# Kernel optimization log

Hardware: AMD Instinct MI355X
Metric: run time of the kernel (lower is better)

## Reference

```python
import jax, jax.numpy as jnp
import numpy as np

B, M, K = 4096, 64, 3          # graphs, points per graph, knn k
FX, FP = 59, 3                 # node features, position dims (FX+FP = 62)
EPS = 1e-5


def _lin_init(key, fan_in, fan_out):
    k1, k2 = jax.random.split(key)
    s = 1.0 / np.sqrt(fan_in)
    W = jax.random.uniform(k1, (fan_in, fan_out), jnp.float32, -s, s)
    b = jax.random.uniform(k2, (fan_out,), jnp.float32, -s, s)
    return W, b


def setup_inputs() -> dict:
    key = jax.random.key(0)
    ks = jax.random.split(key, 8)
    x = jax.random.normal(ks[0], (B * M, FX), jnp.float32)
    pos = jax.random.normal(ks[1], (B * M, FP), jnp.float32)
    batch = jnp.repeat(jnp.arange(B, dtype=jnp.int32), M)
    W1, b1 = _lin_init(ks[2], FX + FP, 128)
    W2, b2 = _lin_init(ks[3], 128, 128)
    Wc1, bc1 = _lin_init(ks[4], 128, 256)
    Wc2, bc2 = _lin_init(ks[5], 256, 1)
    return dict(
        x=x, pos=pos, batch=batch,
        W1=W1, b1=b1, g1=jnp.ones(128), be1=jnp.zeros(128),
        W2=W2, b2=b2, g2=jnp.ones(128), be2=jnp.zeros(128),
        Wc1=Wc1, bc1=bc1, gc1=jnp.ones(256), bec1=jnp.zeros(256),
        Wc2=Wc2, bc2=bc2, gc2=jnp.ones(1), bec2=jnp.zeros(1),
    )


def _mlp_block(h, W, b, g, be):
    # Linear -> ReLU -> BatchNorm1d (training-mode batch statistics)
    h = jax.nn.relu(h @ W + b)
    mu = h.mean(axis=0)
    var = h.var(axis=0)  # biased, as torch BN uses for normalization
    return g * (h - mu) * jax.lax.rsqrt(var + EPS) + be


def _knn_idx(pos_b):
    # pos_b: [B, M, FP]; per-graph k-NN (loop=False)
    d = jnp.sum((pos_b[:, :, None, :] - pos_b[:, None, :, :]) ** 2, axis=-1)  # [B,M,M]
    d = d + jnp.eye(M, dtype=d.dtype) * 1e10  # exclude self-loops
    _, nbr = jax.lax.top_k(-d, K)  # [B, M, K] neighbor (source) indices
    return nbr


def reference(x, pos, batch, W1, b1, g1, be1, W2, b2, g2, be2,
              Wc1, bc1, gc1, bec1, Wc2, bc2, gc2, bec2):
    x_b = x.reshape(B, M, FX)
    pos_b = pos.reshape(B, M, FP)
    nbr = _knn_idx(pos_b)                                   # [B,M,K]
    # gather neighbor features and relative positions (edge messages)
    xj = jax.vmap(lambda xb, nb: xb[nb])(x_b, nbr)          # [B,M,K,FX]
    pj = jax.vmap(lambda pb, nb: pb[nb])(pos_b, nbr)        # [B,M,K,FP]
    rel = pj - pos_b[:, :, None, :]
    msg = jnp.concatenate([xj, rel], axis=-1).reshape(B * M * K, FX + FP)
    # local_nn on every edge, then max aggregation per target node
    h = _mlp_block(msg, W1, b1, g1, be1)                    # [E,128]
    h = h.reshape(B, M, K, 128).max(axis=2).reshape(B * M, 128)
    # global_nn per node
    h = _mlp_block(h, W2, b2, g2, be2)                      # [N,128]
    # global mean pool over graphs
    sums = jax.ops.segment_sum(h, batch, num_segments=B)
    cnt = jax.ops.segment_sum(jnp.ones((B * M,), h.dtype), batch, num_segments=B)
    pooled = sums / cnt[:, None]                            # [B,128]
    # classifier MLP([128,256,1])
    c = _mlp_block(pooled, Wc1, bc1, gc1, bec1)
    c = _mlp_block(c, Wc2, bc2, gc2, bec2)                  # [B,1]
    return jax.nn.sigmoid(c)[:, 0]
```

## Files before the change

### kernel.cpp

```cpp
#include <hip/hip_runtime.h>
#include <hip/hip_bf16.h>
#include <math.h>

#define NB   4096
#define MM   64
#define KNN  3
#define FX   59
#define H    128
#define NN   (NB*MM)
#define NE   (NN*KNN)
#define C1   256
#define EPSB 1e-5f
#define NSH  16

typedef __attribute__((ext_vector_type(8))) short short8;
typedef __attribute__((ext_vector_type(4))) float f32x4;

__device__ __forceinline__ float wave_red(float v) {
#pragma unroll
    for (int m = 32; m >= 1; m >>= 1) v += __shfl_xor(v, m, 64);
    return v;
}

__device__ __forceinline__ void atomAddF(float* p, float v) {
    __hip_atomic_fetch_add(p, v, __ATOMIC_RELAXED, __HIP_MEMORY_SCOPE_AGENT);
}

__device__ __forceinline__ unsigned short f2bf(float f) {
    union { float f; unsigned u; } v; v.f = f;
    unsigned r = v.u + 0x7fffu + ((v.u >> 16) & 1u);
    return (unsigned short)(r >> 16);
}

__device__ __forceinline__ unsigned int pack_bf2(float a, float b) {
    union { __hip_bfloat162 h; unsigned int u; } cv;
    cv.h = __float22bfloat162_rn(make_float2(a, b));
    return cv.u;
}

__global__ __launch_bounds__(512, 8) void k_knn_mfma1(
    const float* __restrict__ x, const float* __restrict__ pos,
    const float* __restrict__ W1, const float* __restrict__ b1,
    unsigned short* __restrict__ h1max,
    float* __restrict__ S1sh, float* __restrict__ Q1sh)
{
    __shared__ float pos_s[MM * 3];
    __shared__ int   nbr_s[MM * 3];
    __shared__ float b1_s[H];
    __shared__ float w1p_s[3 * H];
    __shared__ __align__(16) unsigned short a_s[MM * 72];
    __shared__ __align__(16) unsigned int   u_s32[MM * 66];

    const int blk = blockIdx.x, tid = threadIdx.x;
    const float* xg = x + (size_t)blk * MM * FX;
    const float* pg = pos + (size_t)blk * MM * 3;

    {
        const int node = tid >> 3, g = tid & 7;
        const int c0g = g * 8;
        float v[8];
#pragma unroll
        for (int i = 0; i < 8; ++i) {
            int cI = c0g + i;
            v[i] = (cI < FX) ? xg[node * FX + cI]
                             : ((cI < 62) ? pg[node * 3 + (cI - FX)] : 0.f);
        }
        uint4 pk;
        pk.x = pack_bf2(v[0], v[1]); pk.y = pack_bf2(v[2], v[3]);
        pk.z = pack_bf2(v[4], v[5]); pk.w = pack_bf2(v[6], v[7]);
        const int gs = (g + node) & 7;
        *(uint4*)(a_s + node * 72 + gs * 8) = pk;
    }
    if (tid < MM * 3) pos_s[tid] = pg[tid];
    if (tid < H) b1_s[tid] = b1[tid];
    if (tid < 3 * H) w1p_s[tid] = W1[(FX + (tid >> 7)) * H + (tid & 127)];

    const int lane = tid & 63;
    const int w    = tid >> 6;
    const int m    = lane & 15;
    const int kg   = lane >> 4;
    const int ch   = w * 16 + m;

    short8 bfr[2];
#pragma unroll
    for (int kc = 0; kc < 2; ++kc) {
        float t8[8];
#pragma unroll
        for (int i = 0; i < 8; ++i) {
            int k = kc * 32 + kg * 8 + i;
            t8[i] = (k < 62) ? W1[k * H + ch] : 0.f;
        }
        uint4 pk;
        pk.x = pack_bf2(t8[0], t8[1]); pk.y = pack_bf2(t8[2], t8[3]);
        pk.z = pack_bf2(t8[4], t8[5]); pk.w = pack_bf2(t8[6], t8[7]);
        bfr[kc] = *(short8*)&pk;
    }
    __syncthreads();

    {
        const int node = tid >> 3, q = tid & 7;
        const float px = pos_s[node * 3 + 0];
        const float py = pos_s[node * 3 + 1];
        const float pz = pos_s[node * 3 + 2];
        float d0 = 1e30f, d1 = 1e30f, d2 = 1e30f;
        int   i0 = 1 << 30, i1 = 1 << 30, i2 = 1 << 30;
        for (int jj = 0; jj < 8; ++jj) {
            int j = q * 8 + jj;
            if (j == node) continue;
            float dx = pos_s[j * 3 + 0] - px;
            float dy = pos_s[j * 3 + 1] - py;
            float dz = pos_s[j * 3 + 2] - pz;
            float d = dx * dx + dy * dy + dz * dz;
            bool b2v = (d < d2) || (d == d2 && j < i2);
            bool b1v = (d < d1) || (d == d1 && j < i1);
            bool b0v = (d < d0) || (d == d0 && j < i0);
            float nd2 = b1v ? d1 : d; int ni2 = b1v ? i1 : j;
            float nd1 = b0v ? d0 : d; int ni1 = b0v ? i0 : j;
            d2 = b2v ? nd2 : d2; i2 = b2v ? ni2 : i2;
            d1 = b1v ? nd1 : d1; i1 = b1v ? ni1 : i1;
            d0 = b0v ? d   : d0; i0 = b0v ? j   : i0;
        }
#pragma unroll
        for (int mq = 1; mq <= 4; mq <<= 1) {
            float e[3]; int f[3];
            e[0] = __shfl_xor(d0, mq, 64); f[0] = __shfl_xor(i0, mq, 64);
            e[1] = __shfl_xor(d1, mq, 64); f[1] = __shfl_xor(i1, mq, 64);
            e[2] = __shfl_xor(d2, mq, 64); f[2] = __shfl_xor(i2, mq, 64);
#pragma unroll
            for (int t3 = 0; t3 < 3; ++t3) {
                float ev = e[t3]; int fv = f[t3];
                bool b2v = (ev < d2) || (ev == d2 && fv < i2);
                bool b1v = (ev < d1) || (ev == d1 && fv < i1);
                bool b0v = (ev < d0) || (ev == d0 && fv < i0);
                float nd2 = b1v ? d1 : ev; int ni2 = b1v ? i1 : fv;
                float nd1 = b0v ? d0 : ev; int ni1 = b0v ? i0 : fv;
                d2 = b2v ? nd2 : d2; i2 = b2v ? ni2 : i2;
                d1 = b1v ? nd1 : d1; i1 = b1v ? ni1 : i1;
                d0 = b0v ? ev  : d0; i0 = b0v ? fv  : i0;
            }
        }
        if (q == 0) {
            nbr_s[node * 3 + 0] = i0;
            nbr_s[node * 3 + 1] = i1;
            nbr_s[node * 3 + 2] = i2;
        }
    }

    f32x4 acc[4];
#pragma unroll
    for (int rt = 0; rt < 4; ++rt) acc[rt] = (f32x4){0.f, 0.f, 0.f, 0.f};

#pragma unroll
    for (int kc = 0; kc < 2; ++kc)
#pragma unroll
        for (int rt = 0; rt < 4; ++rt) {
            const int row = rt * 16 + m;
            const int gs = ((kc * 4 + kg) + row) & 7;
            short8 a = *(const short8*)(a_s + row * 72 + gs * 8);
            acc[rt] = __builtin_amdgcn_mfma_f32_16x16x32_bf16(bfr[kc], a, acc[rt], 0, 0, 0);
        }
#pragma unroll
    for (int rt = 0; rt < 4; ++rt) {
        int node = rt * 16 + m;
        int pidx = 8 * w + 2 * kg;
        uint2 val;
        val.x = pack_bf2(acc[rt][0], acc[rt][1]);
        val.y = pack_bf2(acc[rt][2], acc[rt][3]);
        *(uint2*)(u_s32 + node * 66 + pidx) = val;
    }
    __syncthreads();

    const int c0 = 2 * lane, c1v = 2 * lane + 1;
    const float wpa0 = w1p_s[c0],      wpa1 = w1p_s[H + c0],  wpa2 = w1p_s[2 * H + c0];
    const float wpb0 = w1p_s[c1v],     wpb1 = w1p_s[H + c1v], wpb2 = w1p_s[2 * H + c1v];
    const float b1a = b1_s[c0], b1b = b1_s[c1v];
    float s0 = 0.f, s1 = 0.f, q0 = 0.f, q1 = 0.f;
    unsigned int* hout32 = (unsigned int*)(h1max + (size_t)blk * MM * H);
#pragma unroll
    for (int ii = 0; ii < 8; ++ii) {
        int node = w * 8 + ii;
        int j0 = nbr_s[node * 3 + 0];
        int j1 = nbr_s[node * 3 + 1];
        int j2 = nbr_s[node * 3 + 2];
        float px = pos_s[node * 3 + 0], py = pos_s[node * 3 + 1], pz = pos_s[node * 3 + 2];
        float basea = b1a - (px * wpa0 + py * wpa1 + pz * wpa2);
        float baseb = b1b - (px * wpb0 + py * wpb1 + pz * wpb2);
        unsigned int v0 = u_s32[j0 * 66 + lane];
        unsigned int v1 = u_s32[j1 * 66 + lane];
        unsigned int v2 = u_s32[j2 * 66 + lane];
        float h0a = fmaxf(__uint_as_float(v0 << 16) + basea, 0.f);
        float h1a = fmaxf(__uint_as_float(v1 << 16) + basea, 0.f);
        float h2a = fmaxf(__uint_as_float(v2 << 16) + basea, 0.f);
        float h0b = fmaxf(__uint_as_float(v0 & 0xffff0000u) + baseb, 0.f);
        float h1b = fmaxf(__uint_as_float(v1 & 0xffff0000u) + baseb, 0.f);
        float h2b = fmaxf(__uint_as_float(v2 & 0xffff0000u) + baseb, 0.f);
        s0 += h0a + h1a + h2a; q0 += h0a * h0a + h1a * h1a + h2a * h2a;
        s1 += h0b + h1b + h2b; q1 += h0b * h0b + h1b * h1b + h2b * h2b;
        float ma = fmaxf(fmaxf(h0a, h1a), h2a);
        float mb = fmaxf(fmaxf(h0b, h1b), h2b);
        hout32[node * 64 + lane] = pack_bf2(ma, mb);
    }
    __syncthreads();

    float* s_red = (float*)a_s;
    float* q_red = (float*)u_s32;
    *(float2*)(s_red + w * 128 + c0) = make_float2(s0, s1);
    *(float2*)(q_red + w * 128 + c0) = make_float2(q0, q1);
    __syncthreads();
    const int sel = blk & (NSH - 1);
    if (tid < 128) {
        float S = 0.f;
#pragma unroll
        for (int ww = 0; ww < 8; ++ww) S += s_red[ww * 128 + tid];
        atomAddF(&S1sh[sel * H + tid], S);
    } else if (tid < 256) {
        int t2 = tid - 128;
        float Q = 0.f;
#pragma unroll
        for (int ww = 0; ww < 8; ++ww) Q += q_red[ww * 128 + t2];
        atomAddF(&Q1sh[sel * H + t2], Q);
    }
}

__global__ __launch_bounds__(128) void k_prep2(
    const float* __restrict__ W2, const float* __restrict__ S1sh,
    const float* __restrict__ Q1sh, const float* __restrict__ g1,
    const float* __restrict__ be1, const float* __restrict__ b2,
    unsigned short* __restrict__ W2t, float* __restrict__ b2p)
{
    const int n = blockIdx.x, k = threadIdx.x;
    float S = 0.f, Q = 0.f;
#pragma unroll
    for (int i = 0; i < NSH; ++i) { S += S1sh[i * H + k]; Q += Q1sh[i * H + k]; }
    float mu  = S * (1.f / (float)NE);
    float var = Q * (1.f / (float)NE) - mu * mu;
    float a   = g1[k] * rsqrtf(var + EPSB);
    float cc  = be1[k] - mu * a;
    float wv  = W2[k * H + n];
    W2t[n * H + k] = f2bf(a * wv);
    float contrib = wave_red(cc * wv);
    __shared__ float red2[2];
    if ((k & 63) == 0) red2[k >> 6] = contrib;
    __syncthreads();
    if (k == 0) b2p[n] = b2[n] + red2[0] + red2[1];
}

__global__ __launch_bounds__(256) void k_mfma2(
    const unsigned short* __restrict__ h1max, const unsigned short* __restrict__ W2t,
    const float* __restrict__ b2p,
    float* __restrict__ graphsum, float* __restrict__ S2sh, float* __restrict__ Q2sh)
{
    __shared__ __align__(16) unsigned short a_s[MM * 136];
    const int blk = blockIdx.x, tid = threadIdx.x;
    const unsigned short* hg = h1max + (size_t)blk * MM * H;
    for (int t = tid; t < MM * H / 8; t += 256) {
        int row = t >> 4, col8 = (t & 15) * 8;
        *(short8*)(a_s + row * 136 + col8) = *(const short8*)(hg + row * H + col8);
    }
    __syncthreads();

    const int lane = tid & 63, w = tid >> 6, wcol = w * 32;
    const int m = lane & 15, kg = lane >> 4;

    short8 bfr[2][4];
#pragma unroll
    for (int ct = 0; ct < 2; ++ct)
#pragma unroll
        for (int kc = 0; kc < 4; ++kc)
            bfr[ct][kc] = *(const short8*)(W2t + (wcol + ct * 16 + m) * H + kc * 32 + kg * 8);

    f32x4 acc[4][2];
#pragma unroll
    for (int rt = 0; rt < 4; ++rt)
#pragma unroll
        for (int ct = 0; ct < 2; ++ct) acc[rt][ct] = (f32x4){0.f, 0.f, 0.f, 0.f};

#pragma unroll
    for (int kc = 0; kc < 4; ++kc)
#pragma unroll
        for (int rt = 0; rt < 4; ++rt) {
            short8 a = *(const short8*)(a_s + (rt * 16 + m) * 136 + kc * 32 + kg * 8);
#pragma unroll
            for (int ct = 0; ct < 2; ++ct)
                acc[rt][ct] = __builtin_amdgcn_mfma_f32_16x16x32_bf16(a, bfr[ct][kc], acc[rt][ct], 0, 0, 0);
        }

    const int sel = blk & (NSH - 1);
#pragma unroll
    for (int ct = 0; ct < 2; ++ct) {
        float bv = b2p[wcol + ct * 16 + m];
        float s = 0.f, q = 0.f;
#pragma unroll
        for (int rt = 0; rt < 4; ++rt)
#pragma unroll
            for (int r = 0; r < 4; ++r) {
                float v = fmaxf(acc[rt][ct][r] + bv, 0.f);
                s += v; q += v * v;
            }
        s += __shfl_xor(s, 16, 64); q += __shfl_xor(q, 16, 64);
        s += __shfl_xor(s, 32, 64); q += __shfl_xor(q, 32, 64);
        if (lane < 16) {
            int col = wcol + ct * 16 + lane;
            graphsum[(size_t)blk * H + col] = s;
            atomAddF(&S2sh[sel * H + col], s);
            atomAddF(&Q2sh[sel * H + col], q);
        }
    }
}

__global__ __launch_bounds__(256) void k_cls1(
    const float* __restrict__ graphsum,
    const float* __restrict__ S2sh, const float* __restrict__ Q2sh,
    const float* __restrict__ g2, const float* __restrict__ be2,
    const float* __restrict__ Wc1, const float* __restrict__ bc1,
    float* __restrict__ c1raw, float* __restrict__ S3, float* __restrict__ Q3)
{
    __shared__ float a2_s[H], c2_s[H];
    const int blk = blockIdx.x, tid = threadIdx.x;
    if (tid < H) {
        float S = 0.f, Q = 0.f;
#pragma unroll
        for (int i = 0; i < NSH; ++i) { S += S2sh[i * H + tid]; Q += Q2sh[i * H + tid]; }
        float mu  = S * (1.f / (float)NN);
        float var = Q * (1.f / (float)NN) - mu * mu;
        float a   = g2[tid] * rsqrtf(var + EPSB);
        a2_s[tid] = a;
        c2_s[tid] = be2[tid] - mu * a;
    }
    __syncthreads();
    __shared__ float pooled_s[16 * H];
    const int g0 = blk * 16;
    for (int t = tid; t < 16 * H; t += 256) {
        int f = t & 127;
        pooled_s[t] = a2_s[f] * (graphsum[(size_t)g0 * H + t] * (1.f / 64.f)) + c2_s[f];
    }
    __syncthreads();
    const int c = tid;
    float acc[16];
    const float bias = bc1[c];
#pragma unroll
    for (int gi = 0; gi < 16; ++gi) acc[gi] = bias;
    for (int f = 0; f < H; ++f) {
        float wv = Wc1[f * C1 + c];
#pragma unroll
        for (int gi = 0; gi < 16; ++gi) acc[gi] += pooled_s[gi * H + f] * wv;
    }
    float s = 0.f, q = 0.f;
#pragma unroll
    for (int gi = 0; gi < 16; ++gi) {
        float h = fmaxf(acc[gi], 0.f);
        c1raw[(size_t)(g0 + gi) * C1 + c] = h;
        s += h; q += h * h;
    }
    atomAddF(&S3[c], s);
    atomAddF(&Q3[c], q);
}

__global__ __launch_bounds__(256) void k_cls2(
    const float* __restrict__ c1raw,
    const float* __restrict__ S3, const float* __restrict__ Q3,
    const float* __restrict__ gc1, const float* __restrict__ bec1,
    const float* __restrict__ Wc2, const float* __restrict__ bc2,
    float* __restrict__ z, float* __restrict__ SzQz)
{
    __shared__ float a3_s[C1], c3_s[C1], w3_s[C1];
    __shared__ float zloc[16];
    const int blk = blockIdx.x, tid = threadIdx.x;
    {
        float S = S3[tid], Q = Q3[tid];
        float mu  = S * (1.f / (float)NB);
        float var = Q * (1.f / (float)NB) - mu * mu;
        float a   = gc1[tid] * rsqrtf(var + EPSB);
        a3_s[tid] = a;
        c3_s[tid] = bec1[tid] - mu * a;
        w3_s[tid] = Wc2[tid];
    }
    __syncthreads();
    const int g0 = blk * 16;
    {
        const int gi = tid >> 4, part = tid & 15;
        const float* crow = c1raw + (size_t)(g0 + gi) * C1 + part * 16;
        float acc3 = 0.f;
#pragma unroll
        for (int i = 0; i < 16; i += 4) {
            float4 cv = *(const float4*)(crow + i);
            int f = part * 16 + i;
            acc3 += (a3_s[f + 0] * cv.x + c3_s[f + 0]) * w3_s[f + 0];
            acc3 += (a3_s[f + 1] * cv.y + c3_s[f + 1]) * w3_s[f + 1];
            acc3 += (a3_s[f + 2] * cv.z + c3_s[f + 2]) * w3_s[f + 2];
            acc3 += (a3_s[f + 3] * cv.w + c3_s[f + 3]) * w3_s[f + 3];
        }
#pragma unroll
        for (int mm = 1; mm <= 8; mm <<= 1) acc3 += __shfl_xor(acc3, mm, 64);
        if (part == 0) zloc[gi] = fmaxf(acc3 + bc2[0], 0.f);
    }
    __syncthreads();
    if (tid < 16) z[g0 + tid] = zloc[tid];
    if (tid == 0) {
        float s = 0.f, q = 0.f;
#pragma unroll
        for (int i = 0; i < 16; ++i) { float zz = zloc[i]; s += zz; q += zz * zz; }
        atomAddF(&SzQz[0], s);
        atomAddF(&SzQz[1], q);
    }
}

__global__ __launch_bounds__(256) void k_final(
    const float* __restrict__ z, const float* __restrict__ SzQz,
    const float* __restrict__ gc2, const float* __restrict__ bec2,
    float* __restrict__ out)
{
    const int g = blockIdx.x * 256 + threadIdx.x;
    float S = SzQz[0], Q = SzQz[1];
    float mu  = S * (1.f / 4096.f);
    float var = Q * (1.f / 4096.f) - mu * mu;
    float a   = gc2[0] * rsqrtf(var + EPSB);
    float cb  = bec2[0] - mu * a;
    float v = a * z[g] + cb;
    out[g] = 1.f / (1.f + expf(-v));
}

extern "C" void kernel_launch(void* const* d_in, const int* in_sizes, int n_in,
                              void* d_out, int out_size, void* d_ws, size_t ws_size,
                              hipStream_t stream)
{
    const float* x    = (const float*)d_in[0];
    const float* pos  = (const float*)d_in[1];
    const float* W1   = (const float*)d_in[3];
    const float* b1   = (const float*)d_in[4];
    const float* g1   = (const float*)d_in[5];
    const float* be1  = (const float*)d_in[6];
    const float* W2   = (const float*)d_in[7];
    const float* b2   = (const float*)d_in[8];
    const float* g2   = (const float*)d_in[9];
    const float* be2  = (const float*)d_in[10];
    const float* Wc1  = (const float*)d_in[11];
    const float* bc1  = (const float*)d_in[12];
    const float* gc1  = (const float*)d_in[13];
    const float* bec1 = (const float*)d_in[14];
    const float* Wc2  = (const float*)d_in[15];
    const float* bc2  = (const float*)d_in[16];
    const float* gc2  = (const float*)d_in[17];
    const float* bec2 = (const float*)d_in[18];
    float* out = (float*)d_out;

    float* ws = (float*)d_ws;
    size_t off = 0;
    auto alloc = [&](size_t n) { float* p = ws + off; off += n; return p; };
    unsigned short* h1max = (unsigned short*)alloc((size_t)NN * H / 2);
    unsigned short* W2t   = (unsigned short*)alloc(128 * 128 / 2);
    float* b2p     = alloc(H);
    float* graphsum= alloc((size_t)NB * H);
    float* c1raw   = alloc((size_t)NB * C1);
    float* zbuf    = alloc(NB);
    const size_t ATOMN = (size_t)4 * NSH * H + 2 * C1 + 2;
    float* atomics = alloc(ATOMN);
    float* S1sh = atomics;
    float* Q1sh = S1sh + NSH * H;
    float* S2sh = Q1sh + NSH * H;
    float* Q2sh = S2sh + NSH * H;
    float* S3   = Q2sh + NSH * H;
    float* Q3   = S3 + C1;
    float* SzQz = Q3 + C1;

    hipMemsetAsync(atomics, 0, ATOMN * sizeof(float), stream);
    k_knn_mfma1<<<dim3(NB), dim3(512), 0, stream>>>(x, pos, W1, b1, h1max, S1sh, Q1sh);
    k_prep2<<<dim3(128), dim3(128), 0, stream>>>(W2, S1sh, Q1sh, g1, be1, b2, W2t, b2p);
    k_mfma2<<<dim3(NB), dim3(256), 0, stream>>>(h1max, W2t, b2p, graphsum, S2sh, Q2sh);
    k_cls1<<<dim3(256), dim3(256), 0, stream>>>(graphsum, S2sh, Q2sh, g2, be2, Wc1, bc1, c1raw, S3, Q3);
    k_cls2<<<dim3(256), dim3(256), 0, stream>>>(c1raw, S3, Q3, gc1, bec1, Wc2, bc2, zbuf, SzQz);
    k_final<<<dim3(16), dim3(256), 0, stream>>>(zbuf, SzQz, gc2, bec2, out);
}
```

Measured before the change: 254.4 us.

## Gather edge rows into LDS and run MFMA per edge instead of per node

```diff
diff --git a/kernel.cpp b/kernel.cpp
--- a/kernel.cpp
+++ b/kernel.cpp
@@ -47,17 +47,15 @@
     __shared__ float pos_s[MM * 3];
     __shared__ int   nbr_s[MM * 3];
     __shared__ float b1_s[H];
-    __shared__ float w1p_s[3 * H];
     __shared__ __align__(16) unsigned short a_s[MM * 72];
-    __shared__ __align__(16) unsigned int   u_s32[MM * 66];
+    __shared__ __align__(16) unsigned short e_s[3 * MM * 72];
 
     const int blk = blockIdx.x, tid = threadIdx.x;
     const float* xg = x + (size_t)blk * MM * FX;
     const float* pg = pos + (size_t)blk * MM * 3;
 
     {
-        const int node = tid >> 3, g = tid & 7;
-        const int c0g = g * 8;
+        const int node = tid >> 3, c0g = (tid & 7) * 8;
         float v[8];
 #pragma unroll
         for (int i = 0; i < 8; ++i) {
@@ -68,12 +66,10 @@
         uint4 pk;
         pk.x = pack_bf2(v[0], v[1]); pk.y = pack_bf2(v[2], v[3]);
         pk.z = pack_bf2(v[4], v[5]); pk.w = pack_bf2(v[6], v[7]);
-        const int gs = (g + node) & 7;
-        *(uint4*)(a_s + node * 72 + gs * 8) = pk;
+        *(uint4*)(a_s + node * 72 + c0g) = pk;
     }
     if (tid < MM * 3) pos_s[tid] = pg[tid];
     if (tid < H) b1_s[tid] = b1[tid];
-    if (tid < 3 * H) w1p_s[tid] = W1[(FX + (tid >> 7)) * H + (tid & 127)];
 
     const int lane = tid & 63;
     const int w    = tid >> 6;
@@ -145,79 +141,96 @@
             nbr_s[node * 3 + 2] = i2;
         }
     }
-
-    f32x4 acc[4];
-#pragma unroll
-    for (int rt = 0; rt < 4; ++rt) acc[rt] = (f32x4){0.f, 0.f, 0.f, 0.f};
-
-#pragma unroll
-    for (int kc = 0; kc < 2; ++kc)
-#pragma unroll
-        for (int rt = 0; rt < 4; ++rt) {
-            const int row = rt * 16 + m;
-            const int gs = ((kc * 4 + kg) + row) & 7;
-            short8 a = *(const short8*)(a_s + row * 72 + gs * 8);
-            acc[rt] = __builtin_amdgcn_mfma_f32_16x16x32_bf16(bfr[kc], a, acc[rt], 0, 0, 0);
-        }
-#pragma unroll
-    for (int rt = 0; rt < 4; ++rt) {
-        int node = rt * 16 + m;
-        int pidx = 8 * w + 2 * kg;
+    __syncthreads();
+
+#pragma unroll
+    for (int it = 0; it < 3; ++it) {
+        const int T = tid + it * 512;
+        const int row = T >> 3, g = T & 7;
+        const int node = row & 63, slot = row >> 6;
+        const int j = nbr_s[node * 3 + slot];
+        if (g < 7) {
+            *(uint4*)(e_s + row * 72 + g * 8) = *(const uint4*)(a_s + j * 72 + g * 8);
+        } else {
+            uint4 v = *(const uint4*)(a_s + j * 72 + 56);
+            float r0 = pos_s[j * 3 + 0] - pos_s[node * 3 + 0];
+            float r1 = pos_s[j * 3 + 1] - pos_s[node * 3 + 1];
+            float r2 = pos_s[j * 3 + 2] - pos_s[node * 3 + 2];
+            v.y = (v.y & 0xffffu) | ((unsigned)f2bf(r0) << 16);
+            v.z = pack_bf2(r1, r2);
+            v.w = 0u;
+            *(uint4*)(e_s + row * 72 + 56) = v;
+        }
+    }
+    __syncthreads();
+
+    const int cb = w * 16 + kg * 4;
+    const float b1v0 = b1_s[cb + 0], b1v1 = b1_s[cb + 1];
+    const float b1v2 = b1_s[cb + 2], b1v3 = b1_s[cb + 3];
+    float s0 = 0.f, s1 = 0.f, s2 = 0.f, s3 = 0.f;
+    float q0 = 0.f, q1 = 0.f, q2 = 0.f, q3 = 0.f;
+    unsigned int* hout32 = (unsigned int*)(h1max + (size_t)blk * MM * H);
+#pragma unroll
+    for (int rt4 = 0; rt4 < 4; ++rt4) {
+        const int node = rt4 * 16 + m;
+        f32x4 acc0 = (f32x4){0.f,0.f,0.f,0.f};
+        f32x4 acc1 = (f32x4){0.f,0.f,0.f,0.f};
+        f32x4 acc2 = (f32x4){0.f,0.f,0.f,0.f};
+#pragma unroll
+        for (int kc = 0; kc < 2; ++kc) {
+            const int ko = kc * 32 + kg * 8;
+            short8 a0 = *(const short8*)(e_s + (node      ) * 72 + ko);
+            short8 a1 = *(const short8*)(e_s + (node +  64) * 72 + ko);
+            short8 a2 = *(const short8*)(e_s + (node + 128) * 72 + ko);
+            acc0 = __builtin_amdgcn_mfma_f32_16x16x32_bf16(bfr[kc], a0, acc0, 0, 0, 0);
+            acc1 = __builtin_amdgcn_mfma_f32_16x16x32_bf16(bfr[kc], a1, acc1, 0, 0, 0);
+            acc2 = __builtin_amdgcn_mfma_f32_16x16x32_bf16(bfr[kc], a2, acc2, 0, 0, 0);
+        }
+        float hm0, hm1, hm2, hm3;
+        {
+            float ha = fmaxf(acc0[0] + b1v0, 0.f), hb = fmaxf(acc1[0] + b1v0, 0.f), hc = fmaxf(acc2[0] + b1v0, 0.f);
+            s0 += ha + hb + hc; q0 += ha * ha + hb * hb + hc * hc; hm0 = fmaxf(fmaxf(ha, hb), hc);
+        }
+        {
+            float ha = fmaxf(acc0[1] + b1v1, 0.f), hb = fmaxf(acc1[1] + b1v1, 0.f), hc = fmaxf(acc2[1] + b1v1, 0.f);
+            s1 += ha + hb + hc; q1 += ha * ha + hb * hb + hc * hc; hm1 = fmaxf(fmaxf(ha, hb), hc);
+        }
+        {
+            float ha = fmaxf(acc0[2] + b1v2, 0.f), hb = fmaxf(acc1[2] + b1v2, 0.f), hc = fmaxf(acc2[2] + b1v2, 0.f);
+            s2 += ha + hb + hc; q2 += ha * ha + hb * hb + hc * hc; hm2 = fmaxf(fmaxf(ha, hb), hc);
+        }
+        {
+            float ha = fmaxf(acc0[3] + b1v3, 0.f), hb = fmaxf(acc1[3] + b1v3, 0.f), hc = fmaxf(acc2[3] + b1v3, 0.f);
+            s3 += ha + hb + hc; q3 += ha * ha + hb * hb + hc * hc; hm3 = fmaxf(fmaxf(ha, hb), hc);
+        }
         uint2 val;
-        val.x = pack_bf2(acc[rt][0], acc[rt][1]);
-        val.y = pack_bf2(acc[rt][2], acc[rt][3]);
-        *(uint2*)(u_s32 + node * 66 + pidx) = val;
-    }
-    __syncthreads();
-
-    const int c0 = 2 * lane, c1v = 2 * lane + 1;
-    const float wpa0 = w1p_s[c0],      wpa1 = w1p_s[H + c0],  wpa2 = w1p_s[2 * H + c0];
-    const float wpb0 = w1p_s[c1v],     wpb1 = w1p_s[H + c1v], wpb2 = w1p_s[2 * H + c1v];
-    const float b1a = b1_s[c0], b1b = b1_s[c1v];
-    float s0 = 0.f, s1 = 0.f, q0 = 0.f, q1 = 0.f;
-    unsigned int* hout32 = (unsigned int*)(h1max + (size_t)blk * MM * H);
-#pragma unroll
-    for (int ii = 0; ii < 8; ++ii) {
-        int node = w * 8 + ii;
-        int j0 = nbr_s[node * 3 + 0];
-        int j1 = nbr_s[node * 3 + 1];
-        int j2 = nbr_s[node * 3 + 2];
-        float px = pos_s[node * 3 + 0], py = pos_s[node * 3 + 1], pz = pos_s[node * 3 + 2];
-        float basea = b1a - (px * wpa0 + py * wpa1 + pz * wpa2);
-        float baseb = b1b - (px * wpb0 + py * wpb1 + pz * wpb2);
-        unsigned int v0 = u_s32[j0 * 66 + lane];
-        unsigned int v1 = u_s32[j1 * 66 + lane];
-        unsigned int v2 = u_s32[j2 * 66 + lane];
-        float h0a = fmaxf(__uint_as_float(v0 << 16) + basea, 0.f);
-        float h1a = fmaxf(__uint_as_float(v1 << 16) + basea, 0.f);
-        float h2a = fmaxf(__uint_as_float(v2 << 16) + basea, 0.f);
-        float h0b = fmaxf(__uint_as_float(v0 & 0xffff0000u) + baseb, 0.f);
-        float h1b = fmaxf(__uint_as_float(v1 & 0xffff0000u) + baseb, 0.f);
-        float h2b = fmaxf(__uint_as_float(v2 & 0xffff0000u) + baseb, 0.f);
-        s0 += h0a + h1a + h2a; q0 += h0a * h0a + h1a * h1a + h2a * h2a;
-        s1 += h0b + h1b + h2b; q1 += h0b * h0b + h1b * h1b + h2b * h2b;
-        float ma = fmaxf(fmaxf(h0a, h1a), h2a);
-        float mb = fmaxf(fmaxf(h0b, h1b), h2b);
-        hout32[node * 64 + lane] = pack_bf2(ma, mb);
-    }
-    __syncthreads();
-
-    float* s_red = (float*)a_s;
-    float* q_red = (float*)u_s32;
-    *(float2*)(s_red + w * 128 + c0) = make_float2(s0, s1);
-    *(float2*)(q_red + w * 128 + c0) = make_float2(q0, q1);
+        val.x = pack_bf2(hm0, hm1);
+        val.y = pack_bf2(hm2, hm3);
+        *(uint2*)(hout32 + node * 64 + w * 8 + kg * 2) = val;
+    }
+    __syncthreads();
+
+    float* red = (float*)e_s;
+    red[(cb + 0) * 16 + m] = s0;
+    red[(cb + 1) * 16 + m] = s1;
+    red[(cb + 2) * 16 + m] = s2;
+    red[(cb + 3) * 16 + m] = s3;
+    red[2048 + (cb + 0) * 16 + m] = q0;
+    red[2048 + (cb + 1) * 16 + m] = q1;
+    red[2048 + (cb + 2) * 16 + m] = q2;
+    red[2048 + (cb + 3) * 16 + m] = q3;
     __syncthreads();
     const int sel = blk & (NSH - 1);
-    if (tid < 128) {
+    if (tid < H) {
         float S = 0.f;
 #pragma unroll
-        for (int ww = 0; ww < 8; ++ww) S += s_red[ww * 128 + tid];
+        for (int mm = 0; mm < 16; ++mm) S += red[tid * 16 + mm];
         atomAddF(&S1sh[sel * H + tid], S);
-    } else if (tid < 256) {
-        int t2 = tid - 128;
+    } else if (tid < 2 * H) {
+        const int t2 = tid - H;
         float Q = 0.f;
 #pragma unroll
-        for (int ww = 0; ww < 8; ++ww) Q += q_red[ww * 128 + t2];
+        for (int mm = 0; mm < 16; ++mm) Q += red[2048 + t2 * 16 + mm];
         atomAddF(&Q1sh[sel * H + t2], Q);
     }
 }
```

New measurement: 234.3 us. 1.09x faster.
